# Kernel optimization log

Hardware: AMD Instinct MI355X
Metric: run time of the kernel (lower is better)

Reference implementation:

```python
import jax, jax.numpy as jnp
import numpy as np

K0 = 16                       # probe slice length (hard-coded in kernel)
TAU = 2.053748910631823       # t-test threshold (|tau| of kernel constant)


def setup_inputs() -> dict:
    key = jax.random.key(0)
    k1, k2, k3 = jax.random.split(key, 3)
    B, DIN, DOUT = 8192, 4096, 4096
    x = jax.random.normal(k1, (B, DIN), dtype=jnp.float32)
    W = jax.random.normal(k2, (DOUT, DIN), dtype=jnp.float32)
    bias = jax.random.normal(k3, (DOUT,), dtype=jnp.float32)
    return {"x": x, "W": W, "bias": bias}


def reference(x, W, bias):
    # --- partial dot over the first K0 columns of K (the probe) ---
    x0 = x[:, :K0]                    # [B, K0]
    w0 = W[:, :K0]                    # [DOUT, K0]
    y1 = x0 @ w0.T                    # [B, DOUT]  sum_k x_k * w_k
    # sum of squared elementwise products: prod_k^2 = x_k^2 * w_k^2
    s2 = (x0 * x0) @ (w0 * w0).T      # [B, DOUT]
    # --- per-(row, column) t-statistic and early-exit decision ---
    tstat = jnp.abs(y1) / jnp.sqrt(s2 / K0)
    passed = tstat < TAU              # True -> column deemed insignificant, zeroed
    # --- full linear (active columns keep full accumulation + bias) ---
    full = x @ W.T + bias[None, :]    # [B, DOUT]
    return jnp.where(passed, 0.0, full)
```

## Files before the change

kernel.cpp:

```cpp
#include <hip/hip_runtime.h>
#include <cstdint>
#include <cstddef>

#define TAU_D 2.053748910631823
#define M_DIM 8192
#define N_DIM 4096
#define K_DIM 4096
#define NIT   32

typedef float f32x4  __attribute__((ext_vector_type(4)));
typedef short bf16x8 __attribute__((ext_vector_type(8)));

typedef __attribute__((address_space(1))) void gvoid_t;
typedef __attribute__((address_space(3))) void lvoid_t;

__device__ __forceinline__ void gload_lds16(const void* g, void* l) {
    __builtin_amdgcn_global_load_lds((const gvoid_t*)g, (lvoid_t*)l, 16, 0, 0);
}

__device__ __forceinline__ unsigned int pack2bf(float lo, float hi) {
    unsigned int ul = __float_as_uint(lo);
    unsigned int uh = __float_as_uint(hi);
    ul = (ul + 0x7FFFu + ((ul >> 16) & 1u)) >> 16;
    uh = (uh + 0x7FFFu + ((uh >> 16) & 1u)) >> 16;
    return ul | (uh << 16);
}

__global__ void cvt_f32_to_bf16(const float4* __restrict__ in,
                                uint2* __restrict__ out, int n4) {
    int i = blockIdx.x * blockDim.x + threadIdx.x;
    const int stride = gridDim.x * blockDim.x;
    for (; i < n4; i += stride) {
        float4 a = in[i];
        uint2 o;
        o.x = pack2bf(a.x, a.y);
        o.y = pack2bf(a.z, a.w);
        out[i] = o;
    }
}

#define BARRIER() do { __builtin_amdgcn_s_barrier(); \
                       asm volatile("" ::: "memory"); } while (0)

__global__ __launch_bounds__(512, 2) void gemm_masked8(
    const unsigned short* __restrict__ Ab,
    const unsigned short* __restrict__ Bb,
    const float* __restrict__ X,
    const float* __restrict__ Wt,
    const float* __restrict__ bias,
    float* __restrict__ out)
{
    __shared__ __align__(16) char lds[131072];

    const int tid  = threadIdx.x;
    const int wave = tid >> 6;
    const int lane = tid & 63;
    const int lr = lane & 15;
    const int lq = lane >> 4;
    const int wm = wave >> 2;
    const int wn = wave & 3;

    const int flat = blockIdx.x;
    const int xcd  = flat & 7;
    const int s    = flat >> 3;
    const int rnd  = s >> 5;
    const int jj   = s & 31;
    const int trow = rnd * 16 + ((xcd >> 2) << 3) + (jj >> 2);
    const int tcol = ((xcd & 3) << 2) + (jj & 3);
    const int rowBase = trow * 256;
    const int colBase = tcol * 256;

    f32x4 acc[8][4];
    #pragma unroll
    for (int i = 0; i < 8; ++i)
        #pragma unroll
        for (int n = 0; n < 4; ++n)
            acc[i][n] = (f32x4){0.f, 0.f, 0.f, 0.f};

    const int srow  = tid >> 3;
    const int sslot = (tid & 7) ^ (srow & 7);
    const unsigned short* aSrc =
        Ab + (size_t)(rowBase + srow) * K_DIM + sslot * 8;
    const unsigned short* bSrc =
        Bb + (size_t)(colBase + srow) * K_DIM + sslot * 8;

    const unsigned R0A = 0, R0B = 32768, R1A = 65536, R1B = 98304;

    auto stageHalfA = [&](int kst, unsigned reg, int h) {
        #pragma unroll
        for (int i = 2 * h; i < 2 * h + 2; ++i)
            gload_lds16(aSrc + (size_t)i * 64 * K_DIM + kst * 64,
                        lds + reg + i * 8192 + wave * 1024);
    };
    auto stageHalfB = [&](int kst, unsigned reg, int h) {
        #pragma unroll
        for (int i = 2 * h; i < 2 * h + 2; ++i)
            gload_lds16(bSrc + (size_t)i * 64 * K_DIM + kst * 64,
                        lds + reg + i * 8192 + wave * 1024);
    };

    const unsigned kk0 = (unsigned)((lq) ^ (lr & 7)) * 16;
    const unsigned kk1 = (unsigned)((4 + lq) ^ (lr & 7)) * 16;
    const unsigned rowA = (unsigned)(wm * 128 + lr) * 128;
    const unsigned rowB = (unsigned)(wn * 64 + lr) * 128;

    stageHalfA(0, R0A, 0); stageHalfA(0, R0A, 1);
    stageHalfB(0, R0B, 0); stageHalfB(0, R0B, 1);
    stageHalfB(1, R1B, 0); stageHalfB(1, R1B, 1);
    asm volatile("s_waitcnt vmcnt(4)" ::: "memory");
    BARRIER();

    bf16x8 aF[4][2];
    bf16x8 bF0[2][2];
    bf16x8 bF1[2][2];

    for (int j = 0; j < NIT; ++j) {
        const int ka = 2 * j;
        const int kb = 2 * j + 1;
        const bool stg = (j + 1 < NIT);

        #pragma unroll
        for (int m = 0; m < 4; ++m) {
            aF[m][0] = *(const bf16x8*)(lds + R0A + rowA + m * 2048 + kk0);
            aF[m][1] = *(const bf16x8*)(lds + R0A + rowA + m * 2048 + kk1);
        }
        #pragma unroll
        for (int n = 0; n < 2; ++n) {
            bF0[n][0] = *(const bf16x8*)(lds + R0B + rowB + n * 2048 + kk0);
            bF0[n][1] = *(const bf16x8*)(lds + R0B + rowB + n * 2048 + kk1);
        }
        stageHalfA(kb, R1A, 0);
        BARRIER();
        __builtin_amdgcn_s_setprio(1);
        #pragma unroll
        for (int m = 0; m < 4; ++m)
            #pragma unroll
            for (int n = 0; n < 2; ++n)
                #pragma unroll
                for (int ks = 0; ks < 2; ++ks)
                    acc[m][n] = __builtin_amdgcn_mfma_f32_16x16x32_bf16(
                        aF[m][ks], bF0[n][ks], acc[m][n], 0, 0, 0);
        __builtin_amdgcn_s_setprio(0);
        BARRIER();

        #pragma unroll
        for (int n = 0; n < 2; ++n) {
            bF1[n][0] = *(const bf16x8*)(lds + R0B + rowB + (2 + n) * 2048 + kk0);
            bF1[n][1] = *(const bf16x8*)(lds + R0B + rowB + (2 + n) * 2048 + kk1);
        }
        stageHalfA(kb, R1A, 1);
        BARRIER();
        __builtin_amdgcn_s_setprio(1);
        #pragma unroll
        for (int m = 0; m < 4; ++m)
            #pragma unroll
            for (int n = 0; n < 2; ++n)
                #pragma unroll
                for (int ks = 0; ks < 2; ++ks)
                    acc[m][2 + n] = __builtin_amdgcn_mfma_f32_16x16x32_bf16(
                        aF[m][ks], bF1[n][ks], acc[m][2 + n], 0, 0, 0);
        __builtin_amdgcn_s_setprio(0);
        BARRIER();

        #pragma unroll
        for (int m = 0; m < 4; ++m) {
            aF[m][0] = *(const bf16x8*)(lds + R0A + rowA + (4 + m) * 2048 + kk0);
            aF[m][1] = *(const bf16x8*)(lds + R0A + rowA + (4 + m) * 2048 + kk1);
        }
        if (stg) stageHalfB(ka + 2, R0B, 0);
        BARRIER();
        __builtin_amdgcn_s_setprio(1);
        #pragma unroll
        for (int m = 0; m < 4; ++m)
            #pragma unroll
            for (int n = 0; n < 2; ++n)
                #pragma unroll
                for (int ks = 0; ks < 2; ++ks)
                    acc[4 + m][2 + n] = __builtin_amdgcn_mfma_f32_16x16x32_bf16(
                        aF[m][ks], bF1[n][ks], acc[4 + m][2 + n], 0, 0, 0);
        __builtin_amdgcn_s_setprio(0);
        BARRIER();

        if (stg) stageHalfB(ka + 2, R0B, 1);
        __builtin_amdgcn_s_setprio(1);
        #pragma unroll
        for (int m = 0; m < 4; ++m)
            #pragma unroll
            for (int n = 0; n < 2; ++n)
                #pragma unroll
                for (int ks = 0; ks < 2; ++ks)
                    acc[4 + m][n] = __builtin_amdgcn_mfma_f32_16x16x32_bf16(
                        aF[m][ks], bF0[n][ks], acc[4 + m][n], 0, 0, 0);
        __builtin_amdgcn_s_setprio(0);
        if (stg) {
            asm volatile("s_waitcnt vmcnt(4)" ::: "memory");
        } else {
            asm volatile("s_waitcnt vmcnt(0)" ::: "memory");
        }
        BARRIER();

        #pragma unroll
        for (int m = 0; m < 4; ++m) {
            aF[m][0] = *(const bf16x8*)(lds + R1A + rowA + m * 2048 + kk0);
            aF[m][1] = *(const bf16x8*)(lds + R1A + rowA + m * 2048 + kk1);
        }
        #pragma unroll
        for (int n = 0; n < 2; ++n) {
            bF0[n][0] = *(const bf16x8*)(lds + R1B + rowB + n * 2048 + kk0);
            bF0[n][1] = *(const bf16x8*)(lds + R1B + rowB + n * 2048 + kk1);
        }
        if (stg) stageHalfA(ka + 2, R0A, 0);
        BARRIER();
        __builtin_amdgcn_s_setprio(1);
        #pragma unroll
        for (int m = 0; m < 4; ++m)
            #pragma unroll
            for (int n = 0; n < 2; ++n)
                #pragma unroll
                for (int ks = 0; ks < 2; ++ks)
                    acc[m][n] = __builtin_amdgcn_mfma_f32_16x16x32_bf16(
                        aF[m][ks], bF0[n][ks], acc[m][n], 0, 0, 0);
        __builtin_amdgcn_s_setprio(0);
        BARRIER();

        #pragma unroll
        for (int n = 0; n < 2; ++n) {
            bF1[n][0] = *(const bf16x8*)(lds + R1B + rowB + (2 + n) * 2048 + kk0);
            bF1[n][1] = *(const bf16x8*)(lds + R1B + rowB + (2 + n) * 2048 + kk1);
        }
        if (stg) stageHalfA(ka + 2, R0A, 1);
        BARRIER();
        __builtin_amdgcn_s_setprio(1);
        #pragma unroll
        for (int m = 0; m < 4; ++m)
            #pragma unroll
            for (int n = 0; n < 2; ++n)
                #pragma unroll
                for (int ks = 0; ks < 2; ++ks)
                    acc[m][2 + n] = __builtin_amdgcn_mfma_f32_16x16x32_bf16(
                        aF[m][ks], bF1[n][ks], acc[m][2 + n], 0, 0, 0);
        __builtin_amdgcn_s_setprio(0);
        BARRIER();

        #pragma unroll
        for (int m = 0; m < 4; ++m) {
            aF[m][0] = *(const bf16x8*)(lds + R1A + rowA + (4 + m) * 2048 + kk0);
            aF[m][1] = *(const bf16x8*)(lds + R1A + rowA + (4 + m) * 2048 + kk1);
        }
        if (stg) stageHalfB(kb + 2, R1B, 0);
        BARRIER();
        __builtin_amdgcn_s_setprio(1);
        #pragma unroll
        for (int m = 0; m < 4; ++m)
            #pragma unroll
            for (int n = 0; n < 2; ++n)
                #pragma unroll
                for (int ks = 0; ks < 2; ++ks)
                    acc[4 + m][2 + n] = __builtin_amdgcn_mfma_f32_16x16x32_bf16(
                        aF[m][ks], bF1[n][ks], acc[4 + m][2 + n], 0, 0, 0);
        __builtin_amdgcn_s_setprio(0);
        BARRIER();

        if (stg) stageHalfB(kb + 2, R1B, 1);
        __builtin_amdgcn_s_setprio(1);
        #pragma unroll
        for (int m = 0; m < 4; ++m)
            #pragma unroll
            for (int n = 0; n < 2; ++n)
                #pragma unroll
                for (int ks = 0; ks < 2; ++ks)
                    acc[4 + m][n] = __builtin_amdgcn_mfma_f32_16x16x32_bf16(
                        aF[m][ks], bF0[n][ks], acc[4 + m][n], 0, 0, 0);
        __builtin_amdgcn_s_setprio(0);
        if (stg)
            asm volatile("s_waitcnt vmcnt(4)" ::: "memory");
        BARRIER();
    }

    __syncthreads();
    float* x0s = (float*)(lds);
    float* w0s = (float*)(lds + 16384);
    #pragma unroll
    for (int i = 0; i < 2; ++i) {
        int idx = tid + i * 512;
        int r = idx >> 2, qq = (idx & 3) << 2;
        *(f32x4*)(x0s + r * 16 + qq) =
            *(const f32x4*)(X + (size_t)(rowBase + r) * K_DIM + qq);
        *(f32x4*)(w0s + r * 16 + qq) =
            *(const f32x4*)(Wt + (size_t)(colBase + r) * K_DIM + qq);
    }
    __syncthreads();

    const float TAU32 = (float)TAU_D;

    #pragma unroll
    for (int np = 0; np < 4; np += 2) {
        float wv[2][16];
        float bv[2];
        #pragma unroll
        for (int e = 0; e < 2; ++e) {
            const int c = wn * 64 + (np + e) * 16 + lr;
            #pragma unroll
            for (int q = 0; q < 4; ++q)
                *(f32x4*)&wv[e][q * 4] = *(const f32x4*)(w0s + c * 16 + q * 4);
            bv[e] = bias[colBase + c];
        }
        #pragma unroll
        for (int mi = 0; mi < 8; ++mi) {
            #pragma unroll
            for (int jr = 0; jr < 4; ++jr) {
                const int rw = wm * 128 + mi * 16 + lq * 4 + jr;
                float xv[16];
                #pragma unroll
                for (int q = 0; q < 4; ++q)
                    *(f32x4*)&xv[q * 4] = *(const f32x4*)(x0s + rw * 16 + q * 4);
                const size_t orow = (size_t)(rowBase + rw) * N_DIM + colBase;
                #pragma unroll
                for (int e = 0; e < 2; ++e) {
                    const int n = np + e;
                    float y1 = 0.f, s2 = 0.f;
                    #pragma unroll
                    for (int k = 0; k < 16; ++k) {
                        float xk = xv[k], wk = wv[e][k];
                        float xx = xk * xk, ww = wk * wk;
                        y1 = fmaf(xk, wk, y1);
                        s2 = fmaf(xx, ww, s2);
                    }
                    float t = fabsf(y1) / sqrtf(s2 * 0.0625f);
                    float v = (t < TAU32) ? 0.0f : (acc[mi][n][jr] + bv[e]);
                    out[orow + wn * 64 + n * 16 + lr] = v;
                }
            }
        }
    }
}

__global__ __launch_bounds__(256, 2) void gemm_masked_fb(
    const float* __restrict__ X, const float* __restrict__ Wt,
    const float* __restrict__ bias, float* __restrict__ out)
{
    __shared__ __align__(16) unsigned short As[128 * 32];
    __shared__ __align__(16) unsigned short Bs[128 * 32];

    const int tid  = threadIdx.x;
    const int wave = tid >> 6;
    const int lane = tid & 63;
    const int rowBase = blockIdx.y * 128;
    const int colBase = blockIdx.x * 128;
    const int wr = wave >> 1;
    const int wc = wave & 1;
    const int lr = lane & 15;
    const int lq = lane >> 4;

    f32x4 acc[4][4];
    #pragma unroll
    for (int m = 0; m < 4; ++m)
        #pragma unroll
        for (int n = 0; n < 4; ++n)
            acc[m][n] = (f32x4){0.f, 0.f, 0.f, 0.f};

    const int srow = tid >> 2;
    const int scol = (tid & 3) * 8;
    const float* afp = X  + (size_t)(rowBase + srow) * K_DIM + scol;
    const float* bfp = Wt + (size_t)(colBase + srow) * K_DIM + scol;

    for (int kt = 0; kt < K_DIM; kt += 32) {
        #pragma unroll
        for (int issue = 0; issue < 2; ++issue) {
            const float* sa = afp + (size_t)issue * 64 * K_DIM;
            const float* sb = bfp + (size_t)issue * 64 * K_DIM;
            float4 a0 = *(const float4*)(sa);
            float4 a1 = *(const float4*)(sa + 4);
            float4 b0 = *(const float4*)(sb);
            float4 b1 = *(const float4*)(sb + 4);
            uint4 pa, pb;
            pa.x = pack2bf(a0.x, a0.y); pa.y = pack2bf(a0.z, a0.w);
            pa.z = pack2bf(a1.x, a1.y); pa.w = pack2bf(a1.z, a1.w);
            pb.x = pack2bf(b0.x, b0.y); pb.y = pack2bf(b0.z, b0.w);
            pb.z = pack2bf(b1.x, b1.y); pb.w = pack2bf(b1.z, b1.w);
            *(uint4*)((char*)As + issue * 4096 + tid * 16) = pa;
            *(uint4*)((char*)Bs + issue * 4096 + tid * 16) = pb;
        }
        afp += 32; bfp += 32;
        __syncthreads();

        bf16x8 af[4], bq[4];
        #pragma unroll
        for (int m = 0; m < 4; ++m)
            af[m] = *(const bf16x8*)(As + (wr * 64 + m * 16 + lr) * 32 + lq * 8);
        #pragma unroll
        for (int n = 0; n < 4; ++n)
            bq[n] = *(const bf16x8*)(Bs + (wc * 64 + n * 16 + lr) * 32 + lq * 8);
        #pragma unroll
        for (int m = 0; m < 4; ++m)
            #pragma unroll
            for (int n = 0; n < 4; ++n)
                acc[m][n] = __builtin_amdgcn_mfma_f32_16x16x32_bf16(
                    af[m], bq[n], acc[m][n], 0, 0, 0);
        __syncthreads();
    }

    float* x0s = (float*)As;
    float* w0s = (float*)Bs;
    #pragma unroll
    for (int i = 0; i < 2; ++i) {
        int idx = tid + i * 256;
        int r = idx >> 2, q = (idx & 3) * 4;
        *(float4*)(x0s + r * 16 + q) =
            *(const float4*)(X + (size_t)(rowBase + r) * K_DIM + q);
        *(float4*)(w0s + r * 16 + q) =
            *(const float4*)(Wt + (size_t)(colBase + r) * K_DIM + q);
    }
    __syncthreads();

    const float TAU32 = (float)TAU_D;
    float wv[4][16];
    float bv[4];
    #pragma unroll
    for (int n = 0; n < 4; ++n) {
        int c = wc * 64 + n * 16 + lr;
        #pragma unroll
        for (int q = 0; q < 4; ++q)
            *(f32x4*)&wv[n][q * 4] = *(const f32x4*)(w0s + c * 16 + q * 4);
        bv[n] = bias[colBase + c];
    }

    #pragma unroll
    for (int m = 0; m < 4; ++m) {
        #pragma unroll
        for (int j = 0; j < 4; ++j) {
            const int r = wr * 64 + m * 16 + lq * 4 + j;
            float xv[16];
            #pragma unroll
            for (int q = 0; q < 4; ++q)
                *(f32x4*)&xv[q * 4] = *(const f32x4*)(x0s + r * 16 + q * 4);
            const size_t orow = (size_t)(rowBase + r) * N_DIM + colBase;
            #pragma unroll
            for (int n = 0; n < 4; ++n) {
                float y1 = 0.f, s2 = 0.f;
                #pragma unroll
                for (int k = 0; k < 16; ++k) {
                    float xk = xv[k];
                    float wk = wv[n][k];
                    float xx = xk * xk;
                    float ww = wk * wk;
                    y1 = fmaf(xk, wk, y1);
                    s2 = fmaf(xx, ww, s2);
                }
                float t = fabsf(y1) / sqrtf(s2 * 0.0625f);
                float v = (t < TAU32) ? 0.0f : (acc[m][n][j] + bv[n]);
                out[orow + wc * 64 + n * 16 + lr] = v;
            }
        }
    }
}

extern "C" void kernel_launch(void* const* d_in, const int* in_sizes, int n_in,
                              void* d_out, int out_size, void* d_ws, size_t ws_size,
                              hipStream_t stream) {
    const float* x    = (const float*)d_in[0];
    const float* W    = (const float*)d_in[1];
    const float* bias = (const float*)d_in[2];
    float* out = (float*)d_out;

    const size_t needA = (size_t)M_DIM * K_DIM * 2;
    const size_t needB = (size_t)N_DIM * K_DIM * 2;

    if (ws_size >= needA + needB) {
        unsigned short* xb = (unsigned short*)d_ws;
        unsigned short* wb = (unsigned short*)((char*)d_ws + needA);
        cvt_f32_to_bf16<<<2048, 256, 0, stream>>>(
            (const float4*)x, (uint2*)xb, (M_DIM * K_DIM) / 4);
        cvt_f32_to_bf16<<<2048, 256, 0, stream>>>(
            (const float4*)W, (uint2*)wb, (N_DIM * K_DIM) / 4);
        dim3 grid((M_DIM / 256) * (N_DIM / 256));
        gemm_masked8<<<grid, 512, 0, stream>>>(xb, wb, x, W, bias, out);
    } else {
        dim3 grid(N_DIM / 128, M_DIM / 128);
        gemm_masked_fb<<<grid, 256, 0, stream>>>(x, W, bias, out);
    }
}
```

Measured before the change: 315.9 us.

## Double-buffer MFMA fragment registers to halve barriers per K-step

Restructures the main GEMM loop so LDS fragment reads for the next MFMA quadrant are issued before the current quadrant's MFMAs. It uses separate register sets (A0/A1, B0R0/B0R1/B1) so reads and compute overlap. Barriers drop from two per quadrant to one, and vmcnt waits are tightened from 4 to 2 to match the new staging order. This raises VGPR pressure under launch_bounds(512,2) and makes the LDS hazard ordering more delicate.

```diff
diff --git a/kernel.cpp b/kernel.cpp
--- a/kernel.cpp
+++ b/kernel.cpp
@@ -39,8 +39,8 @@
     }
 }
 
-#define BARRIER() do { __builtin_amdgcn_s_barrier(); \
-                       asm volatile("" ::: "memory"); } while (0)
+#define BAR() do { __builtin_amdgcn_s_barrier(); \
+                   asm volatile("" ::: "memory"); } while (0)
 
 __global__ __launch_bounds__(512, 2) void gemm_masked8(
     const unsigned short* __restrict__ Ab,
@@ -104,177 +104,127 @@
     const unsigned rowA = (unsigned)(wm * 128 + lr) * 128;
     const unsigned rowB = (unsigned)(wn * 64 + lr) * 128;
 
+    bf16x8 A0[4][2];
+    bf16x8 A1[4][2];
+    bf16x8 B0R0[2][2];
+    bf16x8 B0R1[2][2];
+    bf16x8 B1[2][2];
+
     stageHalfA(0, R0A, 0); stageHalfA(0, R0A, 1);
     stageHalfB(0, R0B, 0); stageHalfB(0, R0B, 1);
     stageHalfB(1, R1B, 0); stageHalfB(1, R1B, 1);
     asm volatile("s_waitcnt vmcnt(4)" ::: "memory");
-    BARRIER();
-
-    bf16x8 aF[4][2];
-    bf16x8 bF0[2][2];
-    bf16x8 bF1[2][2];
+    __builtin_amdgcn_s_barrier();
+    asm volatile("" ::: "memory");
+    #pragma unroll
+    for (int m = 0; m < 4; ++m) {
+        A0[m][0] = *(const bf16x8*)(lds + R0A + rowA + m * 2048 + kk0);
+        A0[m][1] = *(const bf16x8*)(lds + R0A + rowA + m * 2048 + kk1);
+    }
+    #pragma unroll
+    for (int n = 0; n < 2; ++n) {
+        B0R0[n][0] = *(const bf16x8*)(lds + R0B + rowB + n * 2048 + kk0);
+        B0R0[n][1] = *(const bf16x8*)(lds + R0B + rowB + n * 2048 + kk1);
+    }
+
+    #define MFMA_QUAD(ACC_M, ACC_N, AREG, BREG)                                \
+        do {                                                                   \
+            __builtin_amdgcn_s_setprio(1);                                     \
+            _Pragma("unroll")                                                  \
+            for (int m = 0; m < 4; ++m)                                        \
+                _Pragma("unroll")                                              \
+                for (int n = 0; n < 2; ++n)                                    \
+                    _Pragma("unroll")                                          \
+                    for (int ks = 0; ks < 2; ++ks)                             \
+                        acc[(ACC_M) + m][(ACC_N) + n] =                        \
+                            __builtin_amdgcn_mfma_f32_16x16x32_bf16(           \
+                                AREG[m][ks], BREG[n][ks],                      \
+                                acc[(ACC_M) + m][(ACC_N) + n], 0, 0, 0);       \
+            __builtin_amdgcn_s_setprio(0);                                     \
+        } while (0)
 
     for (int j = 0; j < NIT; ++j) {
         const int ka = 2 * j;
         const int kb = 2 * j + 1;
         const bool stg = (j + 1 < NIT);
 
+        BAR();
+        #pragma unroll
+        for (int n = 0; n < 2; ++n) {
+            B1[n][0] = *(const bf16x8*)(lds + R0B + rowB + (2 + n) * 2048 + kk0);
+            B1[n][1] = *(const bf16x8*)(lds + R0B + rowB + (2 + n) * 2048 + kk1);
+        }
+        stageHalfA(kb, R1A, 0);
+        MFMA_QUAD(0, 0, A0, B0R0);
+
+        BAR();
         #pragma unroll
         for (int m = 0; m < 4; ++m) {
-            aF[m][0] = *(const bf16x8*)(lds + R0A + rowA + m * 2048 + kk0);
-            aF[m][1] = *(const bf16x8*)(lds + R0A + rowA + m * 2048 + kk1);
+            A1[m][0] = *(const bf16x8*)(lds + R0A + rowA + (4 + m) * 2048 + kk0);
+            A1[m][1] = *(const bf16x8*)(lds + R0A + rowA + (4 + m) * 2048 + kk1);
+        }
+        stageHalfA(kb, R1A, 1);
+        MFMA_QUAD(0, 2, A0, B1);
+
+        BAR();
+        if (stg) stageHalfB(ka + 2, R0B, 0);
+        MFMA_QUAD(4, 2, A1, B1);
+        if (stg) asm volatile("s_waitcnt vmcnt(2)" ::: "memory");
+        else     asm volatile("s_waitcnt vmcnt(0)" ::: "memory");
+
+        BAR();
+        #pragma unroll
+        for (int m = 0; m < 4; ++m) {
+            A0[m][0] = *(const bf16x8*)(lds + R1A + rowA + m * 2048 + kk0);
+            A0[m][1] = *(const bf16x8*)(lds + R1A + rowA + m * 2048 + kk1);
         }
         #pragma unroll
         for (int n = 0; n < 2; ++n) {
-            bF0[n][0] = *(const bf16x8*)(lds + R0B + rowB + n * 2048 + kk0);
-            bF0[n][1] = *(const bf16x8*)(lds + R0B + rowB + n * 2048 + kk1);
-        }
-        stageHalfA(kb, R1A, 0);
-        BARRIER();
-        __builtin_amdgcn_s_setprio(1);
-        #pragma unroll
-        for (int m = 0; m < 4; ++m)
-            #pragma unroll
-            for (int n = 0; n < 2; ++n)
-                #pragma unroll
-                for (int ks = 0; ks < 2; ++ks)
-                    acc[m][n] = __builtin_amdgcn_mfma_f32_16x16x32_bf16(
-                        aF[m][ks], bF0[n][ks], acc[m][n], 0, 0, 0);
-        __builtin_amdgcn_s_setprio(0);
-        BARRIER();
-
+            B0R1[n][0] = *(const bf16x8*)(lds + R1B + rowB + n * 2048 + kk0);
+            B0R1[n][1] = *(const bf16x8*)(lds + R1B + rowB + n * 2048 + kk1);
+        }
+        if (stg) stageHalfB(ka + 2, R0B, 1);
+        MFMA_QUAD(4, 0, A1, B0R0);
+
+        BAR();
         #pragma unroll
         for (int n = 0; n < 2; ++n) {
-            bF1[n][0] = *(const bf16x8*)(lds + R0B + rowB + (2 + n) * 2048 + kk0);
-            bF1[n][1] = *(const bf16x8*)(lds + R0B + rowB + (2 + n) * 2048 + kk1);
-        }
-        stageHalfA(kb, R1A, 1);
-        BARRIER();
-        __builtin_amdgcn_s_setprio(1);
-        #pragma unroll
-        for (int m = 0; m < 4; ++m)
-            #pragma unroll
-            for (int n = 0; n < 2; ++n)
-                #pragma unroll
-                for (int ks = 0; ks < 2; ++ks)
-                    acc[m][2 + n] = __builtin_amdgcn_mfma_f32_16x16x32_bf16(
-                        aF[m][ks], bF1[n][ks], acc[m][2 + n], 0, 0, 0);
-        __builtin_amdgcn_s_setprio(0);
-        BARRIER();
-
+            B1[n][0] = *(const bf16x8*)(lds + R1B + rowB + (2 + n) * 2048 + kk0);
+            B1[n][1] = *(const bf16x8*)(lds + R1B + rowB + (2 + n) * 2048 + kk1);
+        }
+        if (stg) stageHalfA(ka + 2, R0A, 0);
+        MFMA_QUAD(0, 0, A0, B0R1);
+
+        BAR();
         #pragma unroll
         for (int m = 0; m < 4; ++m) {
-            aF[m][0] = *(const bf16x8*)(lds + R0A + rowA + (4 + m) * 2048 + kk0);
-            aF[m][1] = *(const bf16x8*)(lds + R0A + rowA + (4 + m) * 2048 + kk1);
-        }
-        if (stg) stageHalfB(ka + 2, R0B, 0);
-        BARRIER();
-        __builtin_amdgcn_s_setprio(1);
-        #pragma unroll
-        for (int m = 0; m < 4; ++m)
-            #pragma unroll
-            for (int n = 0; n < 2; ++n)
-                #pragma unroll
-                for (int ks = 0; ks < 2; ++ks)
-                    acc[4 + m][2 + n] = __builtin_amdgcn_mfma_f32_16x16x32_bf16(
-                        aF[m][ks], bF1[n][ks], acc[4 + m][2 + n], 0, 0, 0);
-        __builtin_amdgcn_s_setprio(0);
-        BARRIER();
-
-        if (stg) stageHalfB(ka + 2, R0B, 1);
-        __builtin_amdgcn_s_setprio(1);
-        #pragma unroll
-        for (int m = 0; m < 4; ++m)
-            #pragma unroll
-            for (int n = 0; n < 2; ++n)
-                #pragma unroll
-                for (int ks = 0; ks < 2; ++ks)
-                    acc[4 + m][n] = __builtin_amdgcn_mfma_f32_16x16x32_bf16(
-                        aF[m][ks], bF0[n][ks], acc[4 + m][n], 0, 0, 0);
-        __builtin_amdgcn_s_setprio(0);
+            A1[m][0] = *(const bf16x8*)(lds + R1A + rowA + (4 + m) * 2048 + kk0);
+            A1[m][1] = *(const bf16x8*)(lds + R1A + rowA + (4 + m) * 2048 + kk1);
+        }
+        if (stg) stageHalfA(ka + 2, R0A, 1);
+        MFMA_QUAD(0, 2, A0, B1);
+
+        BAR();
+        if (stg) stageHalfB(kb + 2, R1B, 0);
+        MFMA_QUAD(4, 2, A1, B1);
+        if (stg) asm volatile("s_waitcnt vmcnt(2)" ::: "memory");
+        else     asm volatile("s_waitcnt vmcnt(0)" ::: "memory");
+
+        BAR();
         if (stg) {
-            asm volatile("s_waitcnt vmcnt(4)" ::: "memory");
-        } else {
-            asm volatile("s_waitcnt vmcnt(0)" ::: "memory");
-        }
-        BARRIER();
-
-        #pragma unroll
-        for (int m = 0; m < 4; ++m) {
-            aF[m][0] = *(const bf16x8*)(lds + R1A + rowA + m * 2048 + kk0);
-            aF[m][1] = *(const bf16x8*)(lds + R1A + rowA + m * 2048 + kk1);
-        }
-        #pragma unroll
-        for (int n = 0; n < 2; ++n) {
-            bF0[n][0] = *(const bf16x8*)(lds + R1B + rowB + n * 2048 + kk0);
-            bF0[n][1] = *(const bf16x8*)(lds + R1B + rowB + n * 2048 + kk1);
-        }
-        if (stg) stageHalfA(ka + 2, R0A, 0);
-        BARRIER();
-        __builtin_amdgcn_s_setprio(1);
-        #pragma unroll
-        for (int m = 0; m < 4; ++m)
-            #pragma unroll
-            for (int n = 0; n < 2; ++n)
-                #pragma unroll
-                for (int ks = 0; ks < 2; ++ks)
-                    acc[m][n] = __builtin_amdgcn_mfma_f32_16x16x32_bf16(
-                        aF[m][ks], bF0[n][ks], acc[m][n], 0, 0, 0);
-        __builtin_amdgcn_s_setprio(0);
-        BARRIER();
-
-        #pragma unroll
-        for (int n = 0; n < 2; ++n) {
-            bF1[n][0] = *(const bf16x8*)(lds + R1B + rowB + (2 + n) * 2048 + kk0);
-            bF1[n][1] = *(const bf16x8*)(lds + R1B + rowB + (2 + n) * 2048 + kk1);
-        }
-        if (stg) stageHalfA(ka + 2, R0A, 1);
-        BARRIER();
-        __builtin_amdgcn_s_setprio(1);
-        #pragma unroll
-        for (int m = 0; m < 4; ++m)
-            #pragma unroll
-            for (int n = 0; n < 2; ++n)
-                #pragma unroll
-                for (int ks = 0; ks < 2; ++ks)
-                    acc[m][2 + n] = __builtin_amdgcn_mfma_f32_16x16x32_bf16(
-                        aF[m][ks], bF1[n][ks], acc[m][2 + n], 0, 0, 0);
-        __builtin_amdgcn_s_setprio(0);
-        BARRIER();
-
-        #pragma unroll
-        for (int m = 0; m < 4; ++m) {
-            aF[m][0] = *(const bf16x8*)(lds + R1A + rowA + (4 + m) * 2048 + kk0);
-            aF[m][1] = *(const bf16x8*)(lds + R1A + rowA + (4 + m) * 2048 + kk1);
-        }
-        if (stg) stageHalfB(kb + 2, R1B, 0);
-        BARRIER();
-        __builtin_amdgcn_s_setprio(1);
-        #pragma unroll
-        for (int m = 0; m < 4; ++m)
-            #pragma unroll
-            for (int n = 0; n < 2; ++n)
-                #pragma unroll
-                for (int ks = 0; ks < 2; ++ks)
-                    acc[4 + m][2 + n] = __builtin_amdgcn_mfma_f32_16x16x32_bf16(
-                        aF[m][ks], bF1[n][ks], acc[4 + m][2 + n], 0, 0, 0);
-        __builtin_amdgcn_s_setprio(0);
-        BARRIER();
-
-        if (stg) stageHalfB(kb + 2, R1B, 1);
-        __builtin_amdgcn_s_setprio(1);
-        #pragma unroll
-        for (int m = 0; m < 4; ++m)
-            #pragma unroll
-            for (int n = 0; n < 2; ++n)
-                #pragma unroll
-                for (int ks = 0; ks < 2; ++ks)
-                    acc[4 + m][n] = __builtin_amdgcn_mfma_f32_16x16x32_bf16(
-                        aF[m][ks], bF0[n][ks], acc[4 + m][n], 0, 0, 0);
-        __builtin_amdgcn_s_setprio(0);
-        if (stg)
-            asm volatile("s_waitcnt vmcnt(4)" ::: "memory");
-        BARRIER();
+            #pragma unroll
+            for (int m = 0; m < 4; ++m) {
+                A0[m][0] = *(const bf16x8*)(lds + R0A + rowA + m * 2048 + kk0);
+                A0[m][1] = *(const bf16x8*)(lds + R0A + rowA + m * 2048 + kk1);
+            }
+            #pragma unroll
+            for (int n = 0; n < 2; ++n) {
+                B0R0[n][0] = *(const bf16x8*)(lds + R0B + rowB + n * 2048 + kk0);
+                B0R0[n][1] = *(const bf16x8*)(lds + R0B + rowB + n * 2048 + kk1);
+            }
+            stageHalfB(kb + 2, R1B, 1);
+        }
+        MFMA_QUAD(4, 0, A1, B0R1);
     }
 
     __syncthreads();
```

Result: slower. 323.3 us (+2.4%).
